# Kernel tuning notes

Hardware: AMD Instinct MI355X
Metric: run time of the kernel (lower is better)

## Reference

```python
import jax, jax.numpy as jnp
import numpy as np
from math import ceil

W, H, L = 1280, 720, 16
NBW = int(ceil(W / L))   # 80
NBH = int(ceil(H / L))   # 45
NUM_BLOCK = NBW * NBH    # 3600
N_POINTS = 32768


def setup_inputs() -> dict:
    key = jax.random.key(0)
    k1, k2 = jax.random.split(key)
    # points uniform over the screen, radii in ~[1, 31] px
    pos2d = jax.random.uniform(k1, (N_POINTS, 2), dtype=jnp.float32) * jnp.array([W, H], dtype=jnp.float32)
    radius = jax.random.uniform(k2, (N_POINTS,), dtype=jnp.float32) * 30.0 + 1.0
    return {"pos2d": pos2d, "radius": radius}


def reference(pos2d, radius):
    # create_tiles: per-point AABB clamped to screen, truncated to int32
    xmin = jnp.clip(pos2d[:, 0] - radius, 0, W).astype(jnp.int32)  # [N]
    ymin = jnp.clip(pos2d[:, 1] - radius, 0, H).astype(jnp.int32)
    xmax = jnp.clip(pos2d[:, 0] + radius, 0, W).astype(jnp.int32)
    ymax = jnp.clip(pos2d[:, 1] + radius, 0, H).astype(jnp.int32)

    # per-tile bounds for all tiles (get_tl / get_br, vectorized)
    ti = jnp.arange(NUM_BLOCK, dtype=jnp.int32)
    xi = ti // NBH
    yi = ti - xi * NBH
    left = xi * L                                   # [T]
    top = yi * L
    right = jnp.minimum((xi + 1) * L, W)
    bottom = jnp.minimum((yi + 1) * L, H)

    # get_inmask for every tile at once -> [T, N] mask
    otl_x = jnp.maximum(xmin[None, :], left[:, None])
    otl_y = jnp.maximum(ymin[None, :], top[:, None])
    obr_x = jnp.minimum(xmax[None, :], right[:, None])
    obr_y = jnp.minimum(ymax[None, :], bottom[:, None])
    in_mask = (obr_x > otl_x) & (obr_y > otl_y)
    return in_mask
```

## Files before the change

### kernel.cpp

```cpp
#include <hip/hip_runtime.h>
#include <hip/hip_bf16.h>

#define SCREEN_W 1280
#define SCREEN_H 720
#define TILE_L   16
#define NBW      80
#define NBH      45
#define NUM_TILE 3600
#define N_POINTS 32768

typedef int v4i __attribute__((ext_vector_type(4)));

__global__ void aabb_kernel(const float* __restrict__ pos2d,
                            const float* __restrict__ radius,
                            unsigned int* __restrict__ pk) {
    int t = blockIdx.x * blockDim.x + threadIdx.x;
    int n = t * 4;
    if (n >= N_POINTS) return;

    const float4* p4 = (const float4*)(pos2d + 2 * n);
    float4 p01 = p4[0];
    float4 p23 = p4[1];
    float4 r   = *(const float4*)(radius + n);

    float xs[4] = {p01.x, p01.z, p23.x, p23.z};
    float ys[4] = {p01.y, p01.w, p23.y, p23.w};
    float rs[4] = {r.x, r.y, r.z, r.w};

    uint4 outp;
    unsigned int* op = &outp.x;
#pragma unroll
    for (int j = 0; j < 4; ++j) {
        float x = xs[j], y = ys[j], rr = rs[j];
        int xmin = (int)fminf(fmaxf(x - rr, 0.0f), (float)SCREEN_W);
        int ymin = (int)fminf(fmaxf(y - rr, 0.0f), (float)SCREEN_H);
        int xmax = (int)fminf(fmaxf(x + rr, 0.0f), (float)SCREEN_W);
        int ymax = (int)fminf(fmaxf(y + rr, 0.0f), (float)SCREEN_H);
        unsigned int ximin = (unsigned int)(xmin >> 4);
        unsigned int ximax = (unsigned int)((xmax + 15) >> 4);
        unsigned int yimin = (unsigned int)(ymin >> 4);
        unsigned int yimax = (unsigned int)((ymax + 15) >> 4);
        op[j] = ximin | (ximax << 8) | (yimin << 16) | (yimax << 24);
    }
    *(uint4*)(pk + n) = outp;
}

__global__ void __launch_bounds__(256)
mask_kernel(const uint4* __restrict__ pk, int* __restrict__ out) {
    int tile = blockIdx.y;
    int t = blockIdx.x * blockDim.x + threadIdx.x;
    int n = t * 4;

    unsigned int xi = (unsigned int)(tile / NBH);
    unsigned int yi = (unsigned int)(tile - (int)xi * NBH);

    uint4 p = pk[t];
    const unsigned int* pp = &p.x;

    v4i res;
#pragma unroll
    for (int j = 0; j < 4; ++j) {
        unsigned int w = pp[j];
        unsigned int ximin =  w        & 0xFFu;
        unsigned int ximax = (w >> 8)  & 0xFFu;
        unsigned int yimin = (w >> 16) & 0xFFu;
        unsigned int yimax =  w >> 24;
        res[j] = (xi >= ximin && xi < ximax && yi >= yimin && yi < yimax) ? 1 : 0;
    }

    *(v4i*)(out + (size_t)tile * N_POINTS + n) = res;
}

extern "C" void kernel_launch(void* const* d_in, const int* in_sizes, int n_in,
                              void* d_out, int out_size, void* d_ws, size_t ws_size,
                              hipStream_t stream) {
    const float* pos2d  = (const float*)d_in[0];
    const float* radius = (const float*)d_in[1];
    int* out = (int*)d_out;
    unsigned int* pk = (unsigned int*)d_ws;

    aabb_kernel<<<dim3(8192 / 256), dim3(256), 0, stream>>>(pos2d, radius, pk);

    mask_kernel<<<dim3(32, NUM_TILE), dim3(256), 0, stream>>>((const uint4*)pk, out);
}
```

Baseline: 446.6 us.

## Replace dense mask evaluation with zero-fill plus per-point tile scatter

Instead of testing every tile against every point, the output is first memset to zero with a grid-stride kernel. A scatter kernel then writes ones only into the tiles covered by each point's bounding box. This aims to make the dense pass a pure store stream, and adds a launch plus scattered stores.

```diff
diff --git a/kernel.cpp b/kernel.cpp
--- a/kernel.cpp
+++ b/kernel.cpp
@@ -46,29 +46,31 @@
 }
 
 __global__ void __launch_bounds__(256)
-mask_kernel(const uint4* __restrict__ pk, int* __restrict__ out) {
-    int tile = blockIdx.y;
-    int t = blockIdx.x * blockDim.x + threadIdx.x;
-    int n = t * 4;
+zero_kernel(v4i* __restrict__ out4) {
+    const int M = NUM_TILE * (N_POINTS / 4);
+    v4i z = {0, 0, 0, 0};
+    int stride = gridDim.x * blockDim.x;
+    for (int i = blockIdx.x * blockDim.x + threadIdx.x; i < M; i += stride)
+        out4[i] = z;
+}
 
-    unsigned int xi = (unsigned int)(tile / NBH);
-    unsigned int yi = (unsigned int)(tile - (int)xi * NBH);
+__global__ void __launch_bounds__(256)
+scatter_kernel(const unsigned int* __restrict__ pk, int* __restrict__ out) {
+    int n = blockIdx.x * blockDim.x + threadIdx.x;
+    if (n >= N_POINTS) return;
 
-    uint4 p = pk[t];
-    const unsigned int* pp = &p.x;
+    unsigned int w = pk[n];
+    unsigned int ximin =  w        & 0xFFu;
+    unsigned int ximax = (w >> 8)  & 0xFFu;
+    unsigned int yimin = (w >> 16) & 0xFFu;
+    unsigned int yimax =  w >> 24;
 
-    v4i res;
-#pragma unroll
-    for (int j = 0; j < 4; ++j) {
-        unsigned int w = pp[j];
-        unsigned int ximin =  w        & 0xFFu;
-        unsigned int ximax = (w >> 8)  & 0xFFu;
-        unsigned int yimin = (w >> 16) & 0xFFu;
-        unsigned int yimax =  w >> 24;
-        res[j] = (xi >= ximin && xi < ximax && yi >= yimin && yi < yimax) ? 1 : 0;
+    for (unsigned int xi = ximin; xi < ximax; ++xi) {
+        int* col = out + ((size_t)(xi * NBH)) * N_POINTS + n;
+        for (unsigned int yi = yimin; yi < yimax; ++yi) {
+            col[(size_t)yi * N_POINTS] = 1;
+        }
     }
-
-    *(v4i*)(out + (size_t)tile * N_POINTS + n) = res;
 }
 
 extern "C" void kernel_launch(void* const* d_in, const int* in_sizes, int n_in,
@@ -81,5 +83,7 @@
 
     aabb_kernel<<<dim3(8192 / 256), dim3(256), 0, stream>>>(pos2d, radius, pk);
 
-    mask_kernel<<<dim3(32, NUM_TILE), dim3(256), 0, stream>>>((const uint4*)pk, out);
+    zero_kernel<<<dim3(2048), dim3(256), 0, stream>>>((v4i*)out);
+
+    scatter_kernel<<<dim3(N_POINTS / 256), dim3(256), 0, stream>>>(pk, out);
 }
```

New measurement: 506.3 us. +13.4%, slower.
